# Performance work log

Hardware: AMD Instinct MI355X
Metric: run time of the kernel (lower is better)

The kernel has to match this reference:

```python
import jax, jax.numpy as jnp
import numpy as np

N = 500_000      # total points
B = 64           # graphs in batch
D_IN = 64        # input feature dim (conv.in_tensor_reps.dim)
D_HID = 128      # EdgeConv MLP hidden
D_OUT = 128      # EdgeConv MLP out


def setup_inputs() -> dict:
    key = jax.random.key(0)
    k = jax.random.split(key, 8)
    x = jax.random.normal(k[0], (N, D_IN), jnp.float32)
    pos = jax.random.normal(k[1], (N, 3), jnp.float32)
    batch = jnp.sort(jax.random.randint(k[2], (N,), 0, B, dtype=jnp.int32))
    lframes = jax.random.normal(k[3], (N, 3, 3), jnp.float32)
    fan1 = 2 * D_IN + 3
    W1 = jax.random.normal(k[4], (fan1, D_HID), jnp.float32) / np.sqrt(fan1)
    b1 = jnp.zeros((D_HID,), jnp.float32)
    W2 = jax.random.normal(k[5], (D_HID, D_OUT), jnp.float32) / np.sqrt(D_HID)
    b2 = jnp.zeros((D_OUT,), jnp.float32)
    return {"x": x, "pos": pos, "batch": batch, "lframes": lframes,
            "W1": W1, "b1": b1, "W2": W2, "b2": b2}


def reference(x, pos, batch, lframes, W1, b1, W2, b2):
    n = pos.shape[0]
    # scatter-mean: center of mass per graph
    counts = jax.ops.segment_sum(jnp.ones((n,), pos.dtype), batch, num_segments=B)
    coms = jax.ops.segment_sum(pos, batch, num_segments=B) / jnp.maximum(counts, 1.0)[:, None]
    # distance of each point to its graph's COM
    dist = jnp.linalg.norm(pos - coms[batch], axis=-1)
    # scatter-min argmin per graph (first occurrence, like torch_scatter.scatter_min)
    min_d = jax.ops.segment_min(dist, batch, num_segments=B)
    node_ids = jnp.arange(n, dtype=jnp.int32)
    cand = jnp.where(dist <= min_d[batch], node_ids, n)
    idx = jnp.minimum(jax.ops.segment_min(cand, batch, num_segments=B), n - 1)  # [B]
    # gathers for the destination (center) nodes
    x_dst = x[idx]          # [B, D_IN]
    pos_dst = pos[idx]      # [B, 3]
    lframes_dst = lframes[idx]  # [B, 3, 3]
    # EdgeConv over edge_index = [arange(N) -> batch]:
    # message_e = MLP([x_dst_i, x_src_j - x_dst_i, pos_j - pos_i]), max-aggregated per graph
    xd = x_dst[batch]                      # [N, D_IN]
    feat = jnp.concatenate([xd, x - xd, pos - pos_dst[batch]], axis=-1)  # [N, 2*D_IN+3]
    h = jax.nn.relu(feat @ W1 + b1)        # [N, D_HID]
    msg = h @ W2 + b2                      # [N, D_OUT]
    out = jax.ops.segment_max(msg, batch, num_segments=B)  # [B, D_OUT]
    return out, pos_dst, batch[idx], lframes_dst
```

## Files before the change

### kernel.cpp

```cpp
#include <hip/hip_runtime.h>
#include <hip/hip_bf16.h>

#define NPTS 500000
#define NGR  64
#define TR   256
#define NT2  ((NPTS + TR - 1) / TR)
#define GRID2 256

typedef __bf16 bf16x8 __attribute__((ext_vector_type(8)));
typedef float f32x4 __attribute__((ext_vector_type(4)));
typedef unsigned int u32x4 __attribute__((ext_vector_type(4)));

#define OFF_BOUNDS 0
#define OFF_OUTACC 6144
#define OFF_CBIAS  38912
#define OFF_W1PT   71680
#define OFF_W1AT   73728
#define OFF_W2T    90112

__device__ __forceinline__ unsigned mapf(float f) {
    union { float f; unsigned u; } v; v.f = f;
    return ((int)v.u >= 0) ? (v.u | 0x80000000u) : ~v.u;
}

#define GLOAD_LDS16(g, l) __builtin_amdgcn_global_load_lds(                 \
    (__attribute__((address_space(1))) void*)(g),                           \
    (__attribute__((address_space(3))) void*)(l), 16, 0, 0)

__global__ void k_prep(const float* __restrict__ W1,
                       const float* __restrict__ W2,
                       const int* __restrict__ batch,
                       unsigned short* __restrict__ W1aT,
                       unsigned short* __restrict__ W2T,
                       float* __restrict__ W1pT,
                       int* __restrict__ bounds,
                       unsigned* __restrict__ outacc) {
    int i = blockIdx.x * 256 + threadIdx.x;
    if (i < 8192) outacc[i] = 0u;
    if (blockIdx.x == 0 && threadIdx.x < 65) {
        int target = threadIdx.x;
        int lo = 0, hi = NPTS;
        while (lo < hi) {
            int mid = (lo + hi) >> 1;
            if (batch[mid] < target) lo = mid + 1; else hi = mid;
        }
        bounds[threadIdx.x] = lo;
    }
    if (i < 8192) {
        int n = i >> 6;
        unsigned short v = (unsigned short)(__builtin_bit_cast(unsigned, (float)(__bf16)W1[(64 + (i & 63)) * 128 + n]) >> 16);
        W1aT[i ^ ((n & 7) << 3)] = v;
    } else if (i < 8192 + 16384) {
        int j = i - 8192; int n = j >> 7, k = j & 127;
        unsigned short v = (unsigned short)(__builtin_bit_cast(unsigned, (float)(__bf16)W2[k * 128 + n]) >> 16);
        W2T[j ^ ((n & 7) << 3)] = v;
    } else if (i < 8192 + 16384 + 512) {
        int j = i - 24576; int n = j >> 2, q = j & 3;
        W1pT[j] = (q < 3) ? W1[(128 + q) * 128 + n] : 0.f;
    }
}

__global__ void k_pre(const float* __restrict__ pos,
                      const int* __restrict__ batch,
                      const float* __restrict__ x,
                      const float* __restrict__ W1,
                      const float* __restrict__ b1,
                      const float* __restrict__ lfr,
                      const int* __restrict__ bounds,
                      float* __restrict__ cbias,
                      float* __restrict__ outf) {
    __shared__ double sd[4][3];
    __shared__ unsigned long long sk[4];
    __shared__ double scom[3];
    __shared__ int sid;
    __shared__ float sposd[3];

    int g = blockIdx.x, t = threadIdx.x;
    int lane = t & 63, wv = t >> 6;
    int s = bounds[g], e = bounds[g + 1];

    double sx = 0.0, sy = 0.0, sz = 0.0;
    for (int i = s + t; i < e; i += 256) {
        sx += (double)pos[i * 3 + 0];
        sy += (double)pos[i * 3 + 1];
        sz += (double)pos[i * 3 + 2];
    }
    #pragma unroll
    for (int m = 1; m < 64; m <<= 1) {
        sx += __shfl_xor(sx, m);
        sy += __shfl_xor(sy, m);
        sz += __shfl_xor(sz, m);
    }
    if (lane == 0) { sd[wv][0] = sx; sd[wv][1] = sy; sd[wv][2] = sz; }
    __syncthreads();
    if (t == 0) {
        double cnt = (double)(e - s);
        double rc = 1.0 / (cnt > 1.0 ? cnt : 1.0);
        scom[0] = (sd[0][0] + sd[1][0] + sd[2][0] + sd[3][0]) * rc;
        scom[1] = (sd[0][1] + sd[1][1] + sd[2][1] + sd[3][1]) * rc;
        scom[2] = (sd[0][2] + sd[1][2] + sd[2][2] + sd[3][2]) * rc;
    }
    __syncthreads();
    double cx = scom[0], cy = scom[1], cz = scom[2];

    unsigned long long key = ~0ULL;
    for (int i = s + t; i < e; i += 256) {
        double dx = (double)pos[i * 3 + 0] - cx;
        double dy = (double)pos[i * 3 + 1] - cy;
        double dz = (double)pos[i * 3 + 2] - cz;
        double d2 = __builtin_fma(dx, dx, __builtin_fma(dy, dy, dz * dz));
        unsigned long long b = __builtin_bit_cast(unsigned long long, d2);
        unsigned long long k2 = (b & ~0xFFFFFULL) | (unsigned long long)i;
        key = k2 < key ? k2 : key;
    }
    #pragma unroll
    for (int m = 1; m < 64; m <<= 1) {
        unsigned long long o = __shfl_xor(key, m);
        key = o < key ? o : key;
    }
    if (lane == 0) sk[wv] = key;
    __syncthreads();
    if (t == 0) {
        unsigned long long k = sk[0];
        if (sk[1] < k) k = sk[1];
        if (sk[2] < k) k = sk[2];
        if (sk[3] < k) k = sk[3];
        int id = (int)(k & 0xFFFFFULL);
        if (id > NPTS - 1) id = NPTS - 1;
        sid = id;
    }
    __syncthreads();
    int id = sid;

    if (t < 3) {
        float p = pos[id * 3 + t];
        sposd[t] = p;
        outf[8192 + g * 3 + t] = p;
    }
    if (t == 4) outf[8192 + 192 + g] = (float)batch[id];
    if (t < 9) outf[8192 + 256 + g * 9 + t] = lfr[id * 9 + t];
    __syncthreads();

    if (t < 128) {
        int c = t;
        float sv = b1[c];
        for (int k = 0; k < 64; ++k) {
            float xd = x[id * 64 + k];
            sv += xd * (W1[k * 128 + c] - W1[(64 + k) * 128 + c]);
        }
        sv -= sposd[0] * W1[128 * 128 + c] + sposd[1] * W1[129 * 128 + c] + sposd[2] * W1[130 * 128 + c];
        cbias[g * 128 + c] = sv;
    }
}

__global__ __launch_bounds__(512, 2) void k_main(
    const float* __restrict__ x,
    const float* __restrict__ pos,
    const int* __restrict__ batch,
    const unsigned short* __restrict__ W1aT,
    const unsigned short* __restrict__ W2T,
    const float* __restrict__ W1pT,
    const float* __restrict__ cbias,
    unsigned* __restrict__ outacc)
{
    __shared__ alignas(16) unsigned char smem[118784];

    const int tid  = threadIdx.x;
    const int w    = tid >> 6;
    const int lane = tid & 63;
    const int quad = lane >> 4;
    const int mr   = lane & 15;

    #pragma unroll
    for (int i = 0; i < 2; ++i)
        GLOAD_LDS16((const char*)W1aT + (i * 512 + tid) * 16,
                    (char*)smem + (i * 512 + tid) * 16);
    #pragma unroll
    for (int i = 0; i < 4; ++i)
        GLOAD_LDS16((const char*)W2T + (i * 512 + tid) * 16,
                    (char*)smem + 16384 + (i * 512 + tid) * 16);

    bf16x8 bfrE[8];
    #pragma unroll
    for (int t8 = 0; t8 < 8; ++t8) {
        f32x4 wp = *(const f32x4*)(W1pT + (t8 * 16 + mr) * 4);
        bf16x8 e = (bf16x8){0, 0, 0, 0, 0, 0, 0, 0};
        if (quad == 0) { e[0] = (__bf16)wp[0]; e[1] = (__bf16)wp[1]; e[2] = (__bf16)wp[2]; }
        bfrE[t8] = e;
    }

    __syncthreads();

    const unsigned short* sW1 = (const unsigned short*)smem;
    const unsigned short* sW2 = (const unsigned short*)(smem + 16384);
    __bf16* hsb = (__bf16*)(smem + 49152) + w * 4352;

    for (int t = blockIdx.x; t < NT2; t += GRID2) {
        const int row0 = t * TR + 32 * w;

        f32x4 av[2][4];
        #pragma unroll
        for (int u = 0; u < 2; ++u) {
            int gr2 = row0 + 16 * u + mr; if (gr2 > NPTS - 1) gr2 = NPTS - 1;
            const float* xp = x + gr2 * 64 + quad * 8;
            av[u][0] = *(const f32x4*)(xp);
            av[u][1] = *(const f32x4*)(xp + 4);
            av[u][2] = *(const f32x4*)(xp + 32);
            av[u][3] = *(const f32x4*)(xp + 36);
        }

        int rowg[2][4]; bool rowv[2][4];
        #pragma unroll
        for (int u = 0; u < 2; ++u)
            #pragma unroll
            for (int r = 0; r < 4; ++r) {
                int gr = row0 + 16 * u + quad * 4 + r;
                rowv[u][r] = (gr < NPTS);
                rowg[u][r] = batch[gr < NPTS ? gr : NPTS - 1];
            }
        int gf = batch[row0 < NPTS ? row0 : NPTS - 1];
        int rl = row0 + 31; if (rl > NPTS - 1) rl = NPTS - 1;
        int gl = batch[rl];
        float cb0[8];
        #pragma unroll
        for (int t8 = 0; t8 < 8; ++t8) cb0[t8] = cbias[gf * 128 + t8 * 16 + mr];
        float pE[2][3];
        #pragma unroll
        for (int u = 0; u < 2; ++u) {
            int gp = row0 + 16 * u + mr; if (gp > NPTS - 1) gp = NPTS - 1;
            pE[u][0] = pos[gp * 3 + 0];
            pE[u][1] = pos[gp * 3 + 1];
            pE[u][2] = pos[gp * 3 + 2];
        }

        bf16x8 afr[2][2];
        #pragma unroll
        for (int u = 0; u < 2; ++u)
            #pragma unroll
            for (int h = 0; h < 2; ++h) {
                f32x4 va = av[u][2 * h], vb = av[u][2 * h + 1];
                bf16x8 a;
                a[0] = (__bf16)va[0]; a[1] = (__bf16)va[1]; a[2] = (__bf16)va[2]; a[3] = (__bf16)va[3];
                a[4] = (__bf16)vb[0]; a[5] = (__bf16)vb[1]; a[6] = (__bf16)vb[2]; a[7] = (__bf16)vb[3];
                afr[u][h] = a;
            }

        f32x4 acc[2][8];
        #pragma unroll
        for (int u = 0; u < 2; ++u)
            #pragma unroll
            for (int t8 = 0; t8 < 8; ++t8) acc[u][t8] = (f32x4){0.f, 0.f, 0.f, 0.f};
        #pragma unroll
        for (int t8 = 0; t8 < 8; ++t8) {
            int n = t8 * 16 + mr;
            int sw = (n & 7) << 3;
            bf16x8 bv0 = __builtin_bit_cast(bf16x8, *(const u32x4*)(sW1 + ((n * 64 + quad * 8) ^ sw)));
            bf16x8 bv1 = __builtin_bit_cast(bf16x8, *(const u32x4*)(sW1 + ((n * 64 + 32 + quad * 8) ^ sw)));
            #pragma unroll
            for (int u = 0; u < 2; ++u) {
                acc[u][t8] = __builtin_amdgcn_mfma_f32_16x16x32_bf16(afr[u][0], bv0, acc[u][t8], 0, 0, 0);
                acc[u][t8] = __builtin_amdgcn_mfma_f32_16x16x32_bf16(afr[u][1], bv1, acc[u][t8], 0, 0, 0);
            }
        }
        bf16x8 aE[2];
        #pragma unroll
        for (int u = 0; u < 2; ++u) {
            bf16x8 a = (bf16x8){0, 0, 0, 0, 0, 0, 0, 0};
            if (quad == 0) { a[0] = (__bf16)pE[u][0]; a[1] = (__bf16)pE[u][1]; a[2] = (__bf16)pE[u][2]; }
            aE[u] = a;
        }
        #pragma unroll
        for (int t8 = 0; t8 < 8; ++t8)
            #pragma unroll
            for (int u = 0; u < 2; ++u)
                acc[u][t8] = __builtin_amdgcn_mfma_f32_16x16x32_bf16(aE[u], bfrE[t8], acc[u][t8], 0, 0, 0);

        #pragma unroll
        for (int u = 0; u < 2; ++u)
            #pragma unroll
            for (int r = 0; r < 4; ++r) {
                int lrow = 16 * u + quad * 4 + r;
                int g = rowg[u][r];
                bool odd = (g != gf);
                #pragma unroll
                for (int t8 = 0; t8 < 8; ++t8) {
                    float cbv = cb0[t8];
                    if (odd) cbv = cbias[g * 128 + t8 * 16 + mr];
                    float v = fmaxf(acc[u][t8][r] + cbv, 0.f);
                    hsb[lrow * 136 + t8 * 16 + mr] = (__bf16)v;
                }
            }

        f32x4 acc2[2][8];
        #pragma unroll
        for (int u = 0; u < 2; ++u)
            #pragma unroll
            for (int t8 = 0; t8 < 8; ++t8) acc2[u][t8] = (f32x4){0.f, 0.f, 0.f, 0.f};
        const unsigned short* hss = (const unsigned short*)hsb;
        #pragma unroll
        for (int kk = 0; kk < 4; ++kk) {
            bf16x8 a2[2];
            #pragma unroll
            for (int u = 0; u < 2; ++u)
                a2[u] = __builtin_bit_cast(bf16x8, *(const u32x4*)(hss + (16 * u + mr) * 136 + kk * 32 + quad * 8));
            #pragma unroll
            for (int t8 = 0; t8 < 8; ++t8) {
                int n = t8 * 16 + mr;
                bf16x8 bv = __builtin_bit_cast(bf16x8, *(const u32x4*)(sW2 + ((n * 128 + kk * 32 + quad * 8) ^ ((n & 7) << 3))));
                #pragma unroll
                for (int u = 0; u < 2; ++u)
                    acc2[u][t8] = __builtin_amdgcn_mfma_f32_16x16x32_bf16(a2[u], bv, acc2[u][t8], 0, 0, 0);
            }
        }

        for (int g = gf; g <= gl; ++g) {
            #pragma unroll
            for (int t8 = 0; t8 < 8; ++t8) {
                float m = -INFINITY;
                #pragma unroll
                for (int u = 0; u < 2; ++u)
                    #pragma unroll
                    for (int r = 0; r < 4; ++r)
                        if (rowv[u][r] && rowg[u][r] == g) m = fmaxf(m, acc2[u][t8][r]);
                m = fmaxf(m, __shfl_xor(m, 16));
                m = fmaxf(m, __shfl_xor(m, 32));
                unsigned mb = __builtin_bit_cast(unsigned, m);
                if (quad == 0 && mb != 0xFF800000u)
                    atomicMax(&outacc[g * 128 + t8 * 16 + mr], mapf(m));
            }
        }
    }
}

__global__ void k_out(const unsigned* __restrict__ outacc,
                      const float* __restrict__ b2v,
                      float* __restrict__ outf) {
    int i = blockIdx.x * 256 + threadIdx.x;
    unsigned key = outacc[i];
    float v;
    if (key == 0u) {
        v = -300.f;
    } else {
        unsigned bits = (key & 0x80000000u) ? (key & 0x7FFFFFFFu) : ~key;
        union { unsigned u; float f; } c; c.u = bits; v = c.f;
    }
    outf[i] = v + b2v[i & 127];
}

extern "C" void kernel_launch(void* const* d_in, const int* in_sizes, int n_in,
                              void* d_out, int out_size, void* d_ws, size_t ws_size,
                              hipStream_t stream) {
    const float* x   = (const float*)d_in[0];
    const float* pos = (const float*)d_in[1];
    const int*   bat = (const int*)d_in[2];
    const float* lfr = (const float*)d_in[3];
    const float* W1  = (const float*)d_in[4];
    const float* b1  = (const float*)d_in[5];
    const float* W2  = (const float*)d_in[6];
    const float* b2v = (const float*)d_in[7];
    float* outf = (float*)d_out;

    char* ws = (char*)d_ws;
    int*            bounds = (int*)(ws + OFF_BOUNDS);
    unsigned*       outacc = (unsigned*)(ws + OFF_OUTACC);
    float*          cbias  = (float*)(ws + OFF_CBIAS);
    float*          W1pT   = (float*)(ws + OFF_W1PT);
    unsigned short* W1aT   = (unsigned short*)(ws + OFF_W1AT);
    unsigned short* W2T    = (unsigned short*)(ws + OFF_W2T);

    k_prep<<<98, 256, 0, stream>>>(W1, W2, bat, W1aT, W2T, W1pT, bounds, outacc);
    k_pre<<<64, 256, 0, stream>>>(pos, bat, x, W1, b1, lfr, bounds, cbias, outf);
    k_main<<<GRID2, 512, 0, stream>>>(x, pos, bat, W1aT, W2T, W1pT, cbias, outacc);
    k_out<<<32, 256, 0, stream>>>(outacc, b2v, outf);
}
```

Before: 278.6 us.

## Read weights from global, shrink LDS, chunk tiles per block, accumulate maxima in registers

The main kernel no longer stages W1/W2 in LDS. It reads the bf16 weight fragments straight from global memory (unswizzled), which cuts the LDS footprint so more blocks fit per CU, and raises the launch bound to 4 blocks. The grid is doubled and each block handles a contiguous chunk of 4 tiles. Per-graph maxima are kept in registers across tiles and flushed with atomics only when the graph changes. The k_pre kernel uses 1024 threads and splits the cbias dot product across 4 partial groups. The cost is repeated global/L2 weight loads inside the MFMA loops in place of LDS reads.

```diff
diff --git a/kernel.cpp b/kernel.cpp
--- a/kernel.cpp
+++ b/kernel.cpp
@@ -5,7 +5,8 @@
 #define NGR  64
 #define TR   256
 #define NT2  ((NPTS + TR - 1) / TR)
-#define GRID2 256
+#define GRID2 512
+#define CHUNK 4
 
 typedef __bf16 bf16x8 __attribute__((ext_vector_type(8)));
 typedef float f32x4 __attribute__((ext_vector_type(4)));
@@ -22,10 +23,6 @@
     union { float f; unsigned u; } v; v.f = f;
     return ((int)v.u >= 0) ? (v.u | 0x80000000u) : ~v.u;
 }
-
-#define GLOAD_LDS16(g, l) __builtin_amdgcn_global_load_lds(                 \
-    (__attribute__((address_space(1))) void*)(g),                           \
-    (__attribute__((address_space(3))) void*)(l), 16, 0, 0)
 
 __global__ void k_prep(const float* __restrict__ W1,
                        const float* __restrict__ W2,
@@ -47,20 +44,19 @@
         bounds[threadIdx.x] = lo;
     }
     if (i < 8192) {
-        int n = i >> 6;
-        unsigned short v = (unsigned short)(__builtin_bit_cast(unsigned, (float)(__bf16)W1[(64 + (i & 63)) * 128 + n]) >> 16);
-        W1aT[i ^ ((n & 7) << 3)] = v;
+        int n = i >> 6, k = i & 63;
+        W1aT[i] = (unsigned short)(__builtin_bit_cast(unsigned, (float)(__bf16)W1[(64 + k) * 128 + n]) >> 16);
     } else if (i < 8192 + 16384) {
         int j = i - 8192; int n = j >> 7, k = j & 127;
-        unsigned short v = (unsigned short)(__builtin_bit_cast(unsigned, (float)(__bf16)W2[k * 128 + n]) >> 16);
-        W2T[j ^ ((n & 7) << 3)] = v;
+        W2T[j] = (unsigned short)(__builtin_bit_cast(unsigned, (float)(__bf16)W2[k * 128 + n]) >> 16);
     } else if (i < 8192 + 16384 + 512) {
         int j = i - 24576; int n = j >> 2, q = j & 3;
         W1pT[j] = (q < 3) ? W1[(128 + q) * 128 + n] : 0.f;
     }
 }
 
-__global__ void k_pre(const float* __restrict__ pos,
+__global__ __launch_bounds__(1024) void k_pre(
+                      const float* __restrict__ pos,
                       const int* __restrict__ batch,
                       const float* __restrict__ x,
                       const float* __restrict__ W1,
@@ -69,18 +65,19 @@
                       const int* __restrict__ bounds,
                       float* __restrict__ cbias,
                       float* __restrict__ outf) {
-    __shared__ double sd[4][3];
-    __shared__ unsigned long long sk[4];
+    __shared__ double sd[16][3];
+    __shared__ unsigned long long sk[16];
     __shared__ double scom[3];
     __shared__ int sid;
     __shared__ float sposd[3];
+    __shared__ float sp[4][128];
 
     int g = blockIdx.x, t = threadIdx.x;
     int lane = t & 63, wv = t >> 6;
     int s = bounds[g], e = bounds[g + 1];
 
     double sx = 0.0, sy = 0.0, sz = 0.0;
-    for (int i = s + t; i < e; i += 256) {
+    for (int i = s + t; i < e; i += 1024) {
         sx += (double)pos[i * 3 + 0];
         sy += (double)pos[i * 3 + 1];
         sz += (double)pos[i * 3 + 2];
@@ -94,17 +91,17 @@
     if (lane == 0) { sd[wv][0] = sx; sd[wv][1] = sy; sd[wv][2] = sz; }
     __syncthreads();
     if (t == 0) {
+        double ax = 0.0, ay = 0.0, az = 0.0;
+        for (int q = 0; q < 16; ++q) { ax += sd[q][0]; ay += sd[q][1]; az += sd[q][2]; }
         double cnt = (double)(e - s);
         double rc = 1.0 / (cnt > 1.0 ? cnt : 1.0);
-        scom[0] = (sd[0][0] + sd[1][0] + sd[2][0] + sd[3][0]) * rc;
-        scom[1] = (sd[0][1] + sd[1][1] + sd[2][1] + sd[3][1]) * rc;
-        scom[2] = (sd[0][2] + sd[1][2] + sd[2][2] + sd[3][2]) * rc;
+        scom[0] = ax * rc; scom[1] = ay * rc; scom[2] = az * rc;
     }
     __syncthreads();
     double cx = scom[0], cy = scom[1], cz = scom[2];
 
     unsigned long long key = ~0ULL;
-    for (int i = s + t; i < e; i += 256) {
+    for (int i = s + t; i < e; i += 1024) {
         double dx = (double)pos[i * 3 + 0] - cx;
         double dy = (double)pos[i * 3 + 1] - cy;
         double dz = (double)pos[i * 3 + 2] - cz;
@@ -122,9 +119,7 @@
     __syncthreads();
     if (t == 0) {
         unsigned long long k = sk[0];
-        if (sk[1] < k) k = sk[1];
-        if (sk[2] < k) k = sk[2];
-        if (sk[3] < k) k = sk[3];
+        for (int q = 1; q < 16; ++q) if (sk[q] < k) k = sk[q];
         int id = (int)(k & 0xFFFFFULL);
         if (id > NPTS - 1) id = NPTS - 1;
         sid = id;
@@ -139,21 +134,28 @@
     }
     if (t == 4) outf[8192 + 192 + g] = (float)batch[id];
     if (t < 9) outf[8192 + 256 + g * 9 + t] = lfr[id * 9 + t];
+
+    if (t < 512) {
+        int c = t & 127, p = t >> 7;
+        float part = 0.f;
+        #pragma unroll
+        for (int kq = 0; kq < 16; ++kq) {
+            int k = p * 16 + kq;
+            float xd = x[id * 64 + k];
+            part += xd * (W1[k * 128 + c] - W1[(64 + k) * 128 + c]);
+        }
+        sp[p][c] = part;
+    }
     __syncthreads();
-
     if (t < 128) {
         int c = t;
-        float sv = b1[c];
-        for (int k = 0; k < 64; ++k) {
-            float xd = x[id * 64 + k];
-            sv += xd * (W1[k * 128 + c] - W1[(64 + k) * 128 + c]);
-        }
+        float sv = b1[c] + sp[0][c] + sp[1][c] + sp[2][c] + sp[3][c];
         sv -= sposd[0] * W1[128 * 128 + c] + sposd[1] * W1[129 * 128 + c] + sposd[2] * W1[130 * 128 + c];
         cbias[g * 128 + c] = sv;
     }
 }
 
-__global__ __launch_bounds__(512, 2) void k_main(
+__global__ __launch_bounds__(512, 4) void k_main(
     const float* __restrict__ x,
     const float* __restrict__ pos,
     const int* __restrict__ batch,
@@ -163,7 +165,7 @@
     const float* __restrict__ cbias,
     unsigned* __restrict__ outacc)
 {
-    __shared__ alignas(16) unsigned char smem[118784];
+    __shared__ alignas(16) unsigned char smem[69632];
 
     const int tid  = threadIdx.x;
     const int w    = tid >> 6;
@@ -171,31 +173,41 @@
     const int quad = lane >> 4;
     const int mr   = lane & 15;
 
-    #pragma unroll
-    for (int i = 0; i < 2; ++i)
-        GLOAD_LDS16((const char*)W1aT + (i * 512 + tid) * 16,
-                    (char*)smem + (i * 512 + tid) * 16);
-    #pragma unroll
-    for (int i = 0; i < 4; ++i)
-        GLOAD_LDS16((const char*)W2T + (i * 512 + tid) * 16,
-                    (char*)smem + 16384 + (i * 512 + tid) * 16);
-
-    bf16x8 bfrE[8];
+    int tb = blockIdx.x * CHUNK;
+    if (tb >= NT2) return;
+    int te = tb + CHUNK; if (te > NT2) te = NT2;
+
+    unsigned ew0[8], ew1[8];
     #pragma unroll
     for (int t8 = 0; t8 < 8; ++t8) {
         f32x4 wp = *(const f32x4*)(W1pT + (t8 * 16 + mr) * 4);
         bf16x8 e = (bf16x8){0, 0, 0, 0, 0, 0, 0, 0};
         if (quad == 0) { e[0] = (__bf16)wp[0]; e[1] = (__bf16)wp[1]; e[2] = (__bf16)wp[2]; }
-        bfrE[t8] = e;
-    }
-
-    __syncthreads();
-
-    const unsigned short* sW1 = (const unsigned short*)smem;
-    const unsigned short* sW2 = (const unsigned short*)(smem + 16384);
-    __bf16* hsb = (__bf16*)(smem + 49152) + w * 4352;
-
-    for (int t = blockIdx.x; t < NT2; t += GRID2) {
+        u32x4 ep = __builtin_bit_cast(u32x4, e);
+        ew0[t8] = ep[0]; ew1[t8] = ep[1];
+    }
+
+    __bf16* hsb = (__bf16*)smem + w * 4352;
+    const unsigned short* hss = (const unsigned short*)hsb;
+
+    int grun = -1;
+    float mcol[8];
+    #pragma unroll
+    for (int t8 = 0; t8 < 8; ++t8) mcol[t8] = -INFINITY;
+
+    auto flushmax = [&](int g) {
+        #pragma unroll
+        for (int t8 = 0; t8 < 8; ++t8) {
+            float m = mcol[t8];
+            m = fmaxf(m, __shfl_xor(m, 16));
+            m = fmaxf(m, __shfl_xor(m, 32));
+            if (quad == 0 && __builtin_bit_cast(unsigned, m) != 0xFF800000u)
+                atomicMax(&outacc[g * 128 + t8 * 16 + mr], mapf(m));
+            mcol[t8] = -INFINITY;
+        }
+    };
+
+    for (int t = tb; t < te; ++t) {
         const int row0 = t * TR + 32 * w;
 
         f32x4 av[2][4];
@@ -252,10 +264,9 @@
             for (int t8 = 0; t8 < 8; ++t8) acc[u][t8] = (f32x4){0.f, 0.f, 0.f, 0.f};
         #pragma unroll
         for (int t8 = 0; t8 < 8; ++t8) {
-            int n = t8 * 16 + mr;
-            int sw = (n & 7) << 3;
-            bf16x8 bv0 = __builtin_bit_cast(bf16x8, *(const u32x4*)(sW1 + ((n * 64 + quad * 8) ^ sw)));
-            bf16x8 bv1 = __builtin_bit_cast(bf16x8, *(const u32x4*)(sW1 + ((n * 64 + 32 + quad * 8) ^ sw)));
+            const u32x4* pbv = (const u32x4*)(W1aT + (t8 * 16 + mr) * 64 + quad * 8);
+            bf16x8 bv0 = __builtin_bit_cast(bf16x8, pbv[0]);
+            bf16x8 bv1 = __builtin_bit_cast(bf16x8, pbv[4]);
             #pragma unroll
             for (int u = 0; u < 2; ++u) {
                 acc[u][t8] = __builtin_amdgcn_mfma_f32_16x16x32_bf16(afr[u][0], bv0, acc[u][t8], 0, 0, 0);
@@ -270,10 +281,13 @@
             aE[u] = a;
         }
         #pragma unroll
-        for (int t8 = 0; t8 < 8; ++t8)
+        for (int t8 = 0; t8 < 8; ++t8) {
+            u32x4 et = (u32x4){ew0[t8], ew1[t8], 0u, 0u};
+            bf16x8 e = __builtin_bit_cast(bf16x8, et);
             #pragma unroll
             for (int u = 0; u < 2; ++u)
-                acc[u][t8] = __builtin_amdgcn_mfma_f32_16x16x32_bf16(aE[u], bfrE[t8], acc[u][t8], 0, 0, 0);
+                acc[u][t8] = __builtin_amdgcn_mfma_f32_16x16x32_bf16(aE[u], e, acc[u][t8], 0, 0, 0);
+        }
 
         #pragma unroll
         for (int u = 0; u < 2; ++u)
@@ -296,7 +310,6 @@
         for (int u = 0; u < 2; ++u)
             #pragma unroll
             for (int t8 = 0; t8 < 8; ++t8) acc2[u][t8] = (f32x4){0.f, 0.f, 0.f, 0.f};
-        const unsigned short* hss = (const unsigned short*)hsb;
         #pragma unroll
         for (int kk = 0; kk < 4; ++kk) {
             bf16x8 a2[2];
@@ -305,31 +318,69 @@
                 a2[u] = __builtin_bit_cast(bf16x8, *(const u32x4*)(hss + (16 * u + mr) * 136 + kk * 32 + quad * 8));
             #pragma unroll
             for (int t8 = 0; t8 < 8; ++t8) {
-                int n = t8 * 16 + mr;
-                bf16x8 bv = __builtin_bit_cast(bf16x8, *(const u32x4*)(sW2 + ((n * 128 + kk * 32 + quad * 8) ^ ((n & 7) << 3))));
+                bf16x8 bv = __builtin_bit_cast(bf16x8, *(const u32x4*)(W2T + (t8 * 16 + mr) * 128 + kk * 32 + quad * 8));
                 #pragma unroll
                 for (int u = 0; u < 2; ++u)
                     acc2[u][t8] = __builtin_amdgcn_mfma_f32_16x16x32_bf16(a2[u], bv, acc2[u][t8], 0, 0, 0);
             }
         }
 
-        for (int g = gf; g <= gl; ++g) {
+        if (gf != grun) {
+            if (grun >= 0) flushmax(grun);
+            grun = gf;
+        }
+        if (gf == gl) {
             #pragma unroll
             for (int t8 = 0; t8 < 8; ++t8) {
-                float m = -INFINITY;
+                float m = mcol[t8];
                 #pragma unroll
                 for (int u = 0; u < 2; ++u)
                     #pragma unroll
                     for (int r = 0; r < 4; ++r)
-                        if (rowv[u][r] && rowg[u][r] == g) m = fmaxf(m, acc2[u][t8][r]);
-                m = fmaxf(m, __shfl_xor(m, 16));
-                m = fmaxf(m, __shfl_xor(m, 32));
-                unsigned mb = __builtin_bit_cast(unsigned, m);
-                if (quad == 0 && mb != 0xFF800000u)
-                    atomicMax(&outacc[g * 128 + t8 * 16 + mr], mapf(m));
-            }
-        }
-    }
+                        if (rowv[u][r]) m = fmaxf(m, acc2[u][t8][r]);
+                mcol[t8] = m;
+            }
+        } else {
+            #pragma unroll
+            for (int t8 = 0; t8 < 8; ++t8) {
+                float m = mcol[t8];
+                #pragma unroll
+                for (int u = 0; u < 2; ++u)
+                    #pragma unroll
+                    for (int r = 0; r < 4; ++r)
+                        if (rowv[u][r] && rowg[u][r] == gf) m = fmaxf(m, acc2[u][t8][r]);
+                mcol[t8] = m;
+            }
+            flushmax(gf);
+            for (int g = gf + 1; g < gl; ++g) {
+                #pragma unroll
+                for (int t8 = 0; t8 < 8; ++t8) {
+                    float m = -INFINITY;
+                    #pragma unroll
+                    for (int u = 0; u < 2; ++u)
+                        #pragma unroll
+                        for (int r = 0; r < 4; ++r)
+                            if (rowv[u][r] && rowg[u][r] == g) m = fmaxf(m, acc2[u][t8][r]);
+                    m = fmaxf(m, __shfl_xor(m, 16));
+                    m = fmaxf(m, __shfl_xor(m, 32));
+                    if (quad == 0 && __builtin_bit_cast(unsigned, m) != 0xFF800000u)
+                        atomicMax(&outacc[g * 128 + t8 * 16 + mr], mapf(m));
+                }
+            }
+            grun = gl;
+            #pragma unroll
+            for (int t8 = 0; t8 < 8; ++t8) {
+                float m = mcol[t8];
+                #pragma unroll
+                for (int u = 0; u < 2; ++u)
+                    #pragma unroll
+                    for (int r = 0; r < 4; ++r)
+                        if (rowv[u][r] && rowg[u][r] == gl) m = fmaxf(m, acc2[u][t8][r]);
+                mcol[t8] = m;
+            }
+        }
+    }
+    if (grun >= 0) flushmax(grun);
 }
 
 __global__ void k_out(const unsigned* __restrict__ outacc,
@@ -369,7 +420,7 @@
     unsigned short* W2T    = (unsigned short*)(ws + OFF_W2T);
 
     k_prep<<<98, 256, 0, stream>>>(W1, W2, bat, W1aT, W2T, W1pT, bounds, outacc);
-    k_pre<<<64, 256, 0, stream>>>(pos, bat, x, W1, b1, lfr, bounds, cbias, outf);
+    k_pre<<<64, 1024, 0, stream>>>(pos, bat, x, W1, b1, lfr, bounds, cbias, outf);
     k_main<<<GRID2, 512, 0, stream>>>(x, pos, bat, W1aT, W2T, W1pT, cbias, outacc);
     k_out<<<32, 256, 0, stream>>>(outacc, b2v, outf);
 }
```

Result: slower. 501.5 us (+80.0%).

## Merge prep kernels, fuse output conversion via last-block flag, restructure main tiling

Applied to the files above, without the earlier changes.

Folds weight transposition and segment-bound search into a 1024-thread k_pre, and moves the final key-to-float conversion into k_main behind a last-block atomic counter, cutting the launch count from four to two. k_main now runs 1024 threads with one 16-row tile per wave, processes contiguous chunks of tiles with the x loads for the next tile prefetched, and reads the position weights from a bf16 LDS copy instead of registers. It also splits the cbias dot product across 512 threads. This trades launch overhead and register pressure against lower MFMA work per wave, a different occupancy, and a grid-wide completion counter.

```diff
diff --git a/kernel.cpp b/kernel.cpp
--- a/kernel.cpp
+++ b/kernel.cpp
@@ -6,17 +6,18 @@
 #define TR   256
 #define NT2  ((NPTS + TR - 1) / TR)
 #define GRID2 256
+#define CHUNK 8
 
 typedef __bf16 bf16x8 __attribute__((ext_vector_type(8)));
 typedef float f32x4 __attribute__((ext_vector_type(4)));
 typedef unsigned int u32x4 __attribute__((ext_vector_type(4)));
 
-#define OFF_BOUNDS 0
+#define OFF_DONE   4096
 #define OFF_OUTACC 6144
 #define OFF_CBIAS  38912
-#define OFF_W1PT   71680
 #define OFF_W1AT   73728
 #define OFF_W2T    90112
+#define OFF_W1ET   122880
 
 __device__ __forceinline__ unsigned mapf(float f) {
     union { float f; unsigned u; } v; v.f = f;
@@ -27,60 +28,66 @@
     (__attribute__((address_space(1))) void*)(g),                           \
     (__attribute__((address_space(3))) void*)(l), 16, 0, 0)
 
-__global__ void k_prep(const float* __restrict__ W1,
-                       const float* __restrict__ W2,
-                       const int* __restrict__ batch,
-                       unsigned short* __restrict__ W1aT,
-                       unsigned short* __restrict__ W2T,
-                       float* __restrict__ W1pT,
-                       int* __restrict__ bounds,
-                       unsigned* __restrict__ outacc) {
-    int i = blockIdx.x * 256 + threadIdx.x;
-    if (i < 8192) outacc[i] = 0u;
-    if (blockIdx.x == 0 && threadIdx.x < 65) {
-        int target = threadIdx.x;
+__global__ __launch_bounds__(1024) void k_pre(
+                      const float* __restrict__ pos,
+                      const int* __restrict__ batch,
+                      const float* __restrict__ x,
+                      const float* __restrict__ W1,
+                      const float* __restrict__ b1,
+                      const float* __restrict__ W2,
+                      const float* __restrict__ lfr,
+                      unsigned short* __restrict__ W1aT,
+                      unsigned short* __restrict__ W2T,
+                      unsigned short* __restrict__ W1eT,
+                      unsigned* __restrict__ outacc,
+                      unsigned* __restrict__ done,
+                      float* __restrict__ cbias,
+                      float* __restrict__ outf) {
+    __shared__ double sd[16][3];
+    __shared__ unsigned long long sk[16];
+    __shared__ double scom[3];
+    __shared__ int sid;
+    __shared__ float sposd[3];
+    __shared__ float sp[4][128];
+    __shared__ int sse[2];
+
+    int g = blockIdx.x, t = threadIdx.x;
+    int lane = t & 63, wv = t >> 6;
+
+    {
+        int i = g * 1024 + t;
+        if (i == 0) *done = 0u;
+        if (i < 8192) {
+            outacc[i] = 0u;
+            int n = i >> 6, k = i & 63;
+            unsigned short v = (unsigned short)(__builtin_bit_cast(unsigned, (float)(__bf16)W1[(64 + k) * 128 + n]) >> 16);
+            W1aT[i ^ ((n & 7) << 3)] = v;
+        } else if (i < 8192 + 16384) {
+            int j = i - 8192; int n = j >> 7, k = j & 127;
+            unsigned short v = (unsigned short)(__builtin_bit_cast(unsigned, (float)(__bf16)W2[k * 128 + n]) >> 16);
+            W2T[j ^ ((n & 7) << 3)] = v;
+        } else if (i < 8192 + 16384 + 4096) {
+            int j = i - 24576; int n = j >> 5, k = j & 31;
+            unsigned short v = 0;
+            if (k < 3) v = (unsigned short)(__builtin_bit_cast(unsigned, (float)(__bf16)W1[(128 + k) * 128 + n]) >> 16);
+            W1eT[j ^ ((n & 3) << 3)] = v;
+        }
+    }
+
+    if (t < 2) {
+        int target = g + t;
         int lo = 0, hi = NPTS;
         while (lo < hi) {
             int mid = (lo + hi) >> 1;
             if (batch[mid] < target) lo = mid + 1; else hi = mid;
         }
-        bounds[threadIdx.x] = lo;
-    }
-    if (i < 8192) {
-        int n = i >> 6;
-        unsigned short v = (unsigned short)(__builtin_bit_cast(unsigned, (float)(__bf16)W1[(64 + (i & 63)) * 128 + n]) >> 16);
-        W1aT[i ^ ((n & 7) << 3)] = v;
-    } else if (i < 8192 + 16384) {
-        int j = i - 8192; int n = j >> 7, k = j & 127;
-        unsigned short v = (unsigned short)(__builtin_bit_cast(unsigned, (float)(__bf16)W2[k * 128 + n]) >> 16);
-        W2T[j ^ ((n & 7) << 3)] = v;
-    } else if (i < 8192 + 16384 + 512) {
-        int j = i - 24576; int n = j >> 2, q = j & 3;
-        W1pT[j] = (q < 3) ? W1[(128 + q) * 128 + n] : 0.f;
-    }
-}
-
-__global__ void k_pre(const float* __restrict__ pos,
-                      const int* __restrict__ batch,
-                      const float* __restrict__ x,
-                      const float* __restrict__ W1,
-                      const float* __restrict__ b1,
-                      const float* __restrict__ lfr,
-                      const int* __restrict__ bounds,
-                      float* __restrict__ cbias,
-                      float* __restrict__ outf) {
-    __shared__ double sd[4][3];
-    __shared__ unsigned long long sk[4];
-    __shared__ double scom[3];
-    __shared__ int sid;
-    __shared__ float sposd[3];
-
-    int g = blockIdx.x, t = threadIdx.x;
-    int lane = t & 63, wv = t >> 6;
-    int s = bounds[g], e = bounds[g + 1];
+        sse[t] = lo;
+    }
+    __syncthreads();
+    int s = sse[0], e = sse[1];
 
     double sx = 0.0, sy = 0.0, sz = 0.0;
-    for (int i = s + t; i < e; i += 256) {
+    for (int i = s + t; i < e; i += 1024) {
         sx += (double)pos[i * 3 + 0];
         sy += (double)pos[i * 3 + 1];
         sz += (double)pos[i * 3 + 2];
@@ -94,17 +101,17 @@
     if (lane == 0) { sd[wv][0] = sx; sd[wv][1] = sy; sd[wv][2] = sz; }
     __syncthreads();
     if (t == 0) {
+        double ax = 0.0, ay = 0.0, az = 0.0;
+        for (int q = 0; q < 16; ++q) { ax += sd[q][0]; ay += sd[q][1]; az += sd[q][2]; }
         double cnt = (double)(e - s);
         double rc = 1.0 / (cnt > 1.0 ? cnt : 1.0);
-        scom[0] = (sd[0][0] + sd[1][0] + sd[2][0] + sd[3][0]) * rc;
-        scom[1] = (sd[0][1] + sd[1][1] + sd[2][1] + sd[3][1]) * rc;
-        scom[2] = (sd[0][2] + sd[1][2] + sd[2][2] + sd[3][2]) * rc;
+        scom[0] = ax * rc; scom[1] = ay * rc; scom[2] = az * rc;
     }
     __syncthreads();
     double cx = scom[0], cy = scom[1], cz = scom[2];
 
     unsigned long long key = ~0ULL;
-    for (int i = s + t; i < e; i += 256) {
+    for (int i = s + t; i < e; i += 1024) {
         double dx = (double)pos[i * 3 + 0] - cx;
         double dy = (double)pos[i * 3 + 1] - cy;
         double dz = (double)pos[i * 3 + 2] - cz;
@@ -122,9 +129,7 @@
     __syncthreads();
     if (t == 0) {
         unsigned long long k = sk[0];
-        if (sk[1] < k) k = sk[1];
-        if (sk[2] < k) k = sk[2];
-        if (sk[3] < k) k = sk[3];
+        for (int q = 1; q < 16; ++q) if (sk[q] < k) k = sk[q];
         int id = (int)(k & 0xFFFFFULL);
         if (id > NPTS - 1) id = NPTS - 1;
         sid = id;
@@ -139,31 +144,40 @@
     }
     if (t == 4) outf[8192 + 192 + g] = (float)batch[id];
     if (t < 9) outf[8192 + 256 + g * 9 + t] = lfr[id * 9 + t];
-    __syncthreads();
-
+
+    if (t < 512) {
+        int c = t & 127, p = t >> 7;
+        float part = 0.f;
+        #pragma unroll
+        for (int kq = 0; kq < 16; ++kq) {
+            int k = p * 16 + kq;
+            float xd = x[id * 64 + k];
+            part += xd * (W1[k * 128 + c] - W1[(64 + k) * 128 + c]);
+        }
+        sp[p][c] = part;
+    }
+    __syncthreads();
     if (t < 128) {
         int c = t;
-        float sv = b1[c];
-        for (int k = 0; k < 64; ++k) {
-            float xd = x[id * 64 + k];
-            sv += xd * (W1[k * 128 + c] - W1[(64 + k) * 128 + c]);
-        }
+        float sv = b1[c] + sp[0][c] + sp[1][c] + sp[2][c] + sp[3][c];
         sv -= sposd[0] * W1[128 * 128 + c] + sposd[1] * W1[129 * 128 + c] + sposd[2] * W1[130 * 128 + c];
         cbias[g * 128 + c] = sv;
     }
 }
 
-__global__ __launch_bounds__(512, 2) void k_main(
+__global__ __launch_bounds__(1024, 1) void k_main(
     const float* __restrict__ x,
     const float* __restrict__ pos,
     const int* __restrict__ batch,
     const unsigned short* __restrict__ W1aT,
-    const unsigned short* __restrict__ W2T,
-    const float* __restrict__ W1pT,
     const float* __restrict__ cbias,
-    unsigned* __restrict__ outacc)
+    unsigned* __restrict__ outacc,
+    unsigned* __restrict__ done,
+    const float* __restrict__ b2v,
+    float* __restrict__ outf)
 {
-    __shared__ alignas(16) unsigned char smem[118784];
+    __shared__ alignas(16) unsigned char smem[124928];
+    __shared__ unsigned sflag;
 
     const int tid  = threadIdx.x;
     const int w    = tid >> 6;
@@ -172,144 +186,115 @@
     const int mr   = lane & 15;
 
     #pragma unroll
-    for (int i = 0; i < 2; ++i)
-        GLOAD_LDS16((const char*)W1aT + (i * 512 + tid) * 16,
-                    (char*)smem + (i * 512 + tid) * 16);
-    #pragma unroll
-    for (int i = 0; i < 4; ++i)
-        GLOAD_LDS16((const char*)W2T + (i * 512 + tid) * 16,
-                    (char*)smem + 16384 + (i * 512 + tid) * 16);
-
-    bf16x8 bfrE[8];
-    #pragma unroll
-    for (int t8 = 0; t8 < 8; ++t8) {
-        f32x4 wp = *(const f32x4*)(W1pT + (t8 * 16 + mr) * 4);
-        bf16x8 e = (bf16x8){0, 0, 0, 0, 0, 0, 0, 0};
-        if (quad == 0) { e[0] = (__bf16)wp[0]; e[1] = (__bf16)wp[1]; e[2] = (__bf16)wp[2]; }
-        bfrE[t8] = e;
-    }
-
+    for (int i = 0; i < 4; ++i) {
+        int c = i * 1024 + tid;
+        if (c < 3584)
+            GLOAD_LDS16((const char*)W1aT + c * 16, (char*)smem + c * 16);
+    }
     __syncthreads();
 
     const unsigned short* sW1 = (const unsigned short*)smem;
-    const unsigned short* sW2 = (const unsigned short*)(smem + 16384);
-    __bf16* hsb = (__bf16*)(smem + 49152) + w * 4352;
-
-    for (int t = blockIdx.x; t < NT2; t += GRID2) {
-        const int row0 = t * TR + 32 * w;
-
-        f32x4 av[2][4];
-        #pragma unroll
-        for (int u = 0; u < 2; ++u) {
-            int gr2 = row0 + 16 * u + mr; if (gr2 > NPTS - 1) gr2 = NPTS - 1;
-            const float* xp = x + gr2 * 64 + quad * 8;
-            av[u][0] = *(const f32x4*)(xp);
-            av[u][1] = *(const f32x4*)(xp + 4);
-            av[u][2] = *(const f32x4*)(xp + 32);
-            av[u][3] = *(const f32x4*)(xp + 36);
-        }
-
-        int rowg[2][4]; bool rowv[2][4];
-        #pragma unroll
-        for (int u = 0; u < 2; ++u)
-            #pragma unroll
-            for (int r = 0; r < 4; ++r) {
-                int gr = row0 + 16 * u + quad * 4 + r;
-                rowv[u][r] = (gr < NPTS);
-                rowg[u][r] = batch[gr < NPTS ? gr : NPTS - 1];
-            }
+    const unsigned short* sW2 = sW1 + 8192;
+    const unsigned short* sWe = sW1 + 24576;
+    __bf16* hsb = (__bf16*)(smem + 57344) + w * 2112;
+    const unsigned short* hss = (const unsigned short*)hsb;
+
+    int tb = blockIdx.x * CHUNK;
+    int te = tb + CHUNK; if (te > NT2) te = NT2;
+
+    f32x4 av[4];
+    if (tb < te) {
+        int gr = tb * TR + 16 * w + mr; if (gr > NPTS - 1) gr = NPTS - 1;
+        const float* xp = x + (size_t)gr * 64 + quad * 8;
+        av[0] = *(const f32x4*)(xp);
+        av[1] = *(const f32x4*)(xp + 4);
+        av[2] = *(const f32x4*)(xp + 32);
+        av[3] = *(const f32x4*)(xp + 36);
+    }
+
+    for (int t = tb; t < te; ++t) {
+        const int row0 = t * TR + 16 * w;
+
+        bf16x8 afr0, afr1;
+        {
+            f32x4 va = av[0], vb = av[1], vc = av[2], vd = av[3];
+            afr0[0] = (__bf16)va[0]; afr0[1] = (__bf16)va[1]; afr0[2] = (__bf16)va[2]; afr0[3] = (__bf16)va[3];
+            afr0[4] = (__bf16)vb[0]; afr0[5] = (__bf16)vb[1]; afr0[6] = (__bf16)vb[2]; afr0[7] = (__bf16)vb[3];
+            afr1[0] = (__bf16)vc[0]; afr1[1] = (__bf16)vc[1]; afr1[2] = (__bf16)vc[2]; afr1[3] = (__bf16)vc[3];
+            afr1[4] = (__bf16)vd[0]; afr1[5] = (__bf16)vd[1]; afr1[6] = (__bf16)vd[2]; afr1[7] = (__bf16)vd[3];
+        }
+        if (t + 1 < te) {
+            int gr = (t + 1) * TR + 16 * w + mr; if (gr > NPTS - 1) gr = NPTS - 1;
+            const float* xp = x + (size_t)gr * 64 + quad * 8;
+            av[0] = *(const f32x4*)(xp);
+            av[1] = *(const f32x4*)(xp + 4);
+            av[2] = *(const f32x4*)(xp + 32);
+            av[3] = *(const f32x4*)(xp + 36);
+        }
+
+        int rowg[4]; bool rowv[4];
+        #pragma unroll
+        for (int r = 0; r < 4; ++r) {
+            int gr = row0 + quad * 4 + r;
+            rowv[r] = (gr < NPTS);
+            rowg[r] = batch[gr < NPTS ? gr : NPTS - 1];
+        }
         int gf = batch[row0 < NPTS ? row0 : NPTS - 1];
-        int rl = row0 + 31; if (rl > NPTS - 1) rl = NPTS - 1;
+        int rl = row0 + 15; if (rl > NPTS - 1) rl = NPTS - 1;
         int gl = batch[rl];
         float cb0[8];
         #pragma unroll
         for (int t8 = 0; t8 < 8; ++t8) cb0[t8] = cbias[gf * 128 + t8 * 16 + mr];
-        float pE[2][3];
-        #pragma unroll
-        for (int u = 0; u < 2; ++u) {
-            int gp = row0 + 16 * u + mr; if (gp > NPTS - 1) gp = NPTS - 1;
-            pE[u][0] = pos[gp * 3 + 0];
-            pE[u][1] = pos[gp * 3 + 1];
-            pE[u][2] = pos[gp * 3 + 2];
-        }
-
-        bf16x8 afr[2][2];
-        #pragma unroll
-        for (int u = 0; u < 2; ++u)
-            #pragma unroll
-            for (int h = 0; h < 2; ++h) {
-                f32x4 va = av[u][2 * h], vb = av[u][2 * h + 1];
-                bf16x8 a;
-                a[0] = (__bf16)va[0]; a[1] = (__bf16)va[1]; a[2] = (__bf16)va[2]; a[3] = (__bf16)va[3];
-                a[4] = (__bf16)vb[0]; a[5] = (__bf16)vb[1]; a[6] = (__bf16)vb[2]; a[7] = (__bf16)vb[3];
-                afr[u][h] = a;
-            }
-
-        f32x4 acc[2][8];
-        #pragma unroll
-        for (int u = 0; u < 2; ++u)
-            #pragma unroll
-            for (int t8 = 0; t8 < 8; ++t8) acc[u][t8] = (f32x4){0.f, 0.f, 0.f, 0.f};
+        bf16x8 aE = (bf16x8){0, 0, 0, 0, 0, 0, 0, 0};
+        {
+            int gp = row0 + mr; if (gp > NPTS - 1) gp = NPTS - 1;
+            if (quad == 0) {
+                aE[0] = (__bf16)pos[gp * 3 + 0];
+                aE[1] = (__bf16)pos[gp * 3 + 1];
+                aE[2] = (__bf16)pos[gp * 3 + 2];
+            }
+        }
+
+        f32x4 acc[8];
+        #pragma unroll
+        for (int t8 = 0; t8 < 8; ++t8) acc[t8] = (f32x4){0.f, 0.f, 0.f, 0.f};
         #pragma unroll
         for (int t8 = 0; t8 < 8; ++t8) {
             int n = t8 * 16 + mr;
             int sw = (n & 7) << 3;
             bf16x8 bv0 = __builtin_bit_cast(bf16x8, *(const u32x4*)(sW1 + ((n * 64 + quad * 8) ^ sw)));
             bf16x8 bv1 = __builtin_bit_cast(bf16x8, *(const u32x4*)(sW1 + ((n * 64 + 32 + quad * 8) ^ sw)));
+            bf16x8 bve = __builtin_bit_cast(bf16x8, *(const u32x4*)(sWe + ((n * 32 + quad * 8) ^ ((n & 3) << 3))));
+            acc[t8] = __builtin_amdgcn_mfma_f32_16x16x32_bf16(afr0, bv0, acc[t8], 0, 0, 0);
+            acc[t8] = __builtin_amdgcn_mfma_f32_16x16x32_bf16(afr1, bv1, acc[t8], 0, 0, 0);
+            acc[t8] = __builtin_amdgcn_mfma_f32_16x16x32_bf16(aE,   bve, acc[t8], 0, 0, 0);
+        }
+
+        #pragma unroll
+        for (int r = 0; r < 4; ++r) {
+            int lrow = quad * 4 + r;
+            int g = rowg[r];
+            bool odd = (g != gf);
             #pragma unroll
-            for (int u = 0; u < 2; ++u) {
-                acc[u][t8] = __builtin_amdgcn_mfma_f32_16x16x32_bf16(afr[u][0], bv0, acc[u][t8], 0, 0, 0);
-                acc[u][t8] = __builtin_amdgcn_mfma_f32_16x16x32_bf16(afr[u][1], bv1, acc[u][t8], 0, 0, 0);
-            }
-        }
-        bf16x8 aE[2];
-        #pragma unroll
-        for (int u = 0; u < 2; ++u) {
-            bf16x8 a = (bf16x8){0, 0, 0, 0, 0, 0, 0, 0};
-            if (quad == 0) { a[0] = (__bf16)pE[u][0]; a[1] = (__bf16)pE[u][1]; a[2] = (__bf16)pE[u][2]; }
-            aE[u] = a;
-        }
-        #pragma unroll
-        for (int t8 = 0; t8 < 8; ++t8)
-            #pragma unroll
-            for (int u = 0; u < 2; ++u)
-                acc[u][t8] = __builtin_amdgcn_mfma_f32_16x16x32_bf16(aE[u], bfrE[t8], acc[u][t8], 0, 0, 0);
-
-        #pragma unroll
-        for (int u = 0; u < 2; ++u)
-            #pragma unroll
-            for (int r = 0; r < 4; ++r) {
-                int lrow = 16 * u + quad * 4 + r;
-                int g = rowg[u][r];
-                bool odd = (g != gf);
-                #pragma unroll
-                for (int t8 = 0; t8 < 8; ++t8) {
-                    float cbv = cb0[t8];
-                    if (odd) cbv = cbias[g * 128 + t8 * 16 + mr];
-                    float v = fmaxf(acc[u][t8][r] + cbv, 0.f);
-                    hsb[lrow * 136 + t8 * 16 + mr] = (__bf16)v;
-                }
-            }
-
-        f32x4 acc2[2][8];
-        #pragma unroll
-        for (int u = 0; u < 2; ++u)
-            #pragma unroll
-            for (int t8 = 0; t8 < 8; ++t8) acc2[u][t8] = (f32x4){0.f, 0.f, 0.f, 0.f};
-        const unsigned short* hss = (const unsigned short*)hsb;
+            for (int t8 = 0; t8 < 8; ++t8) {
+                float cbv = cb0[t8];
+                if (odd) cbv = cbias[g * 128 + t8 * 16 + mr];
+                float v = fmaxf(acc[t8][r] + cbv, 0.f);
+                hsb[lrow * 132 + t8 * 16 + mr] = (__bf16)v;
+            }
+        }
+
+        f32x4 acc2[8];
+        #pragma unroll
+        for (int t8 = 0; t8 < 8; ++t8) acc2[t8] = (f32x4){0.f, 0.f, 0.f, 0.f};
         #pragma unroll
         for (int kk = 0; kk < 4; ++kk) {
-            bf16x8 a2[2];
-            #pragma unroll
-            for (int u = 0; u < 2; ++u)
-                a2[u] = __builtin_bit_cast(bf16x8, *(const u32x4*)(hss + (16 * u + mr) * 136 + kk * 32 + quad * 8));
+            bf16x8 a2 = __builtin_bit_cast(bf16x8, *(const u32x4*)(hss + mr * 132 + kk * 32 + quad * 8));
             #pragma unroll
             for (int t8 = 0; t8 < 8; ++t8) {
                 int n = t8 * 16 + mr;
                 bf16x8 bv = __builtin_bit_cast(bf16x8, *(const u32x4*)(sW2 + ((n * 128 + kk * 32 + quad * 8) ^ ((n & 7) << 3))));
-                #pragma unroll
-                for (int u = 0; u < 2; ++u)
-                    acc2[u][t8] = __builtin_amdgcn_mfma_f32_16x16x32_bf16(a2[u], bv, acc2[u][t8], 0, 0, 0);
+                acc2[t8] = __builtin_amdgcn_mfma_f32_16x16x32_bf16(a2, bv, acc2[t8], 0, 0, 0);
             }
         }
 
@@ -318,33 +303,33 @@
             for (int t8 = 0; t8 < 8; ++t8) {
                 float m = -INFINITY;
                 #pragma unroll
-                for (int u = 0; u < 2; ++u)
-                    #pragma unroll
-                    for (int r = 0; r < 4; ++r)
-                        if (rowv[u][r] && rowg[u][r] == g) m = fmaxf(m, acc2[u][t8][r]);
+                for (int r = 0; r < 4; ++r)
+                    if (rowv[r] && rowg[r] == g) m = fmaxf(m, acc2[t8][r]);
                 m = fmaxf(m, __shfl_xor(m, 16));
                 m = fmaxf(m, __shfl_xor(m, 32));
-                unsigned mb = __builtin_bit_cast(unsigned, m);
-                if (quad == 0 && mb != 0xFF800000u)
+                if (quad == 0 && __builtin_bit_cast(unsigned, m) != 0xFF800000u)
                     atomicMax(&outacc[g * 128 + t8 * 16 + mr], mapf(m));
             }
         }
     }
-}
-
-__global__ void k_out(const unsigned* __restrict__ outacc,
-                      const float* __restrict__ b2v,
-                      float* __restrict__ outf) {
-    int i = blockIdx.x * 256 + threadIdx.x;
-    unsigned key = outacc[i];
-    float v;
-    if (key == 0u) {
-        v = -300.f;
-    } else {
-        unsigned bits = (key & 0x80000000u) ? (key & 0x7FFFFFFFu) : ~key;
-        union { unsigned u; float f; } c; c.u = bits; v = c.f;
-    }
-    outf[i] = v + b2v[i & 127];
+
+    __threadfence();
+    __syncthreads();
+    if (tid == 0) sflag = atomicAdd(done, 1u);
+    __syncthreads();
+    if (sflag == (unsigned)(gridDim.x - 1)) {
+        for (int i = tid; i < 8192; i += 1024) {
+            unsigned key = atomicMax(&outacc[i], 0u);
+            float v;
+            if (key == 0u) {
+                v = -300.f;
+            } else {
+                unsigned bits = (key & 0x80000000u) ? (key & 0x7FFFFFFFu) : ~key;
+                union { unsigned u; float f; } c; c.u = bits; v = c.f;
+            }
+            outf[i] = v + b2v[i & 127];
+        }
+    }
 }
 
 extern "C" void kernel_launch(void* const* d_in, const int* in_sizes, int n_in,
@@ -361,15 +346,14 @@
     float* outf = (float*)d_out;
 
     char* ws = (char*)d_ws;
-    int*            bounds = (int*)(ws + OFF_BOUNDS);
+    unsigned*       done   = (unsigned*)(ws + OFF_DONE);
     unsigned*       outacc = (unsigned*)(ws + OFF_OUTACC);
     float*          cbias  = (float*)(ws + OFF_CBIAS);
-    float*          W1pT   = (float*)(ws + OFF_W1PT);
     unsigned short* W1aT   = (unsigned short*)(ws + OFF_W1AT);
     unsigned short* W2T    = (unsigned short*)(ws + OFF_W2T);
-
-    k_prep<<<98, 256, 0, stream>>>(W1, W2, bat, W1aT, W2T, W1pT, bounds, outacc);
-    k_pre<<<64, 256, 0, stream>>>(pos, bat, x, W1, b1, lfr, bounds, cbias, outf);
-    k_main<<<GRID2, 512, 0, stream>>>(x, pos, bat, W1aT, W2T, W1pT, cbias, outacc);
-    k_out<<<32, 256, 0, stream>>>(outacc, b2v, outf);
+    unsigned short* W1eT   = (unsigned short*)(ws + OFF_W1ET);
+
+    k_pre<<<64, 1024, 0, stream>>>(pos, bat, x, W1, b1, W2, lfr,
+                                   W1aT, W2T, W1eT, outacc, done, cbias, outf);
+    k_main<<<GRID2, 1024, 0, stream>>>(x, pos, bat, W1aT, cbias, outacc, done, b2v, outf);
 }
```

Result: slower. 354.7 us (+27.3%).
